# Kernel tuning notes

Measured on AMD Instinct MI355X. Metric: run time of the kernel, lower is better.

The kernel has to match this reference:

```python
import jax, jax.numpy as jnp
import numpy as np

H = 32  # rnn/encoder/residual hidden dim
NEG = -1e9


def gru(x, h0, Wih, Whh, bih, bhh):
    # x: (B,T,D), h0: (B,H); torch GRU gate order [r,z,n]
    xp = jnp.swapaxes(x @ Wih.T + bih, 0, 1)  # (T,B,3H)

    def step(h, xt):
        gh = h @ Whh.T + bhh
        xr, xz, xn = jnp.split(xt, 3, axis=-1)
        hr, hz, hn = jnp.split(gh, 3, axis=-1)
        r = jax.nn.sigmoid(xr + hr)
        z = jax.nn.sigmoid(xz + hz)
        n = jnp.tanh(xn + r * hn)
        h_new = (1.0 - z) * n + z * h
        return h_new, h_new

    hT, ys = jax.lax.scan(step, h0, xp)
    return jnp.swapaxes(ys, 0, 1), hT  # (B,T,H), (B,H)


def setup_inputs():
    key = jax.random.key(0)
    ks = jax.random.split(key, 30)
    B, T = 2048, 128
    def lin(k, o, i):
        return jax.random.normal(k, (o, i), jnp.float32) / np.sqrt(i)
    inp = {}
    inp['obs'] = jax.random.normal(ks[0], (B, T, 15), jnp.float32)
    inp['rnn_state'] = jax.random.normal(ks[1], (1, B, 3 * H), jnp.float32)
    inp['enc_air_W'] = lin(ks[2], H, 7); inp['enc_air_b'] = jnp.zeros((H,), jnp.float32)
    inp['enc_m_W'] = lin(ks[3], H, 4); inp['enc_m_b'] = jnp.zeros((H,), jnp.float32)
    inp['air_Wih'] = lin(ks[4], 3 * H, H); inp['air_Whh'] = lin(ks[5], 3 * H, H)
    inp['air_bih'] = jnp.zeros((3 * H,), jnp.float32); inp['air_bhh'] = jnp.zeros((3 * H,), jnp.float32)
    inp['m_Wih'] = lin(ks[6], 3 * H, H); inp['m_Whh'] = lin(ks[7], 3 * H, H)
    inp['m_bih'] = jnp.zeros((3 * H,), jnp.float32); inp['m_bhh'] = jnp.zeros((3 * H,), jnp.float32)
    inp['attn_in_w'] = lin(ks[8], 3 * H, H); inp['attn_in_b'] = jnp.zeros((3 * H,), jnp.float32)
    inp['attn_out_w'] = lin(ks[9], H, H); inp['attn_out_b'] = jnp.zeros((H,), jnp.float32)
    inp['mlp_W0'] = lin(ks[10], 256, 2 * H); inp['mlp_b0'] = jnp.zeros((256,), jnp.float32)
    inp['mlp_W1'] = lin(ks[11], 256, 256); inp['mlp_b1'] = jnp.zeros((256,), jnp.float32)
    inp['out_W'] = lin(ks[12], 1, 256); inp['out_b'] = jnp.zeros((1,), jnp.float32)
    return inp


def reference(obs, rnn_state, enc_air_W, enc_air_b, enc_m_W, enc_m_b,
              air_Wih, air_Whh, air_bih, air_bhh,
              m_Wih, m_Whh, m_bih, m_bhh,
              attn_in_w, attn_in_b, attn_out_w, attn_out_b,
              mlp_W0, mlp_b0, mlp_W1, mlp_b1, out_W, out_b):
    B, T, _ = obs.shape
    h_air0 = rnn_state[0, :, :H]                       # (B,H)
    h_m0 = rnn_state[0, :, H:].reshape(2 * B, H)       # faithful reshape (1,B,64)->(1,2B,32)

    # aircraft branch
    air_emb = obs[..., 8:] @ enc_air_W.T + enc_air_b   # (B,T,H)
    air_feat, next_h_air = gru(air_emb, h_air0, air_Wih, air_Whh, air_bih, air_bhh)

    # missile branch: concat missiles along batch dim
    m_raw = jnp.concatenate([obs[..., 0:4], obs[..., 4:8]], axis=0)  # (2B,T,4)
    m_emb = m_raw @ enc_m_W.T + enc_m_b
    m_feat, next_h_m = gru(m_emb, h_m0, m_Wih, m_Whh, m_bih, m_bhh)
    m1_feat, m2_feat = m_feat[:B], m_feat[B:]

    # inactive-missile mask from raw obs
    obs_flat = obs.reshape(-1, 15)
    inact = jnp.array([1.0, 0.0, 1.0, 0.0], jnp.float32)
    mask = jnp.stack([
        jnp.all(jnp.isclose(obs_flat[:, 0:4], inact), axis=-1),
        jnp.all(jnp.isclose(obs_flat[:, 4:8], inact), axis=-1),
    ], axis=1)                                          # (N,2) True = masked

    N = B * T
    air_flat = air_feat.reshape(N, H)
    m1_flat = m1_feat.reshape(N, H)
    m2_flat = m2_feat.reshape(N, H)

    # 2-head attention, q len 1, kv len 2
    Wq, Wk, Wv = jnp.split(attn_in_w, 3, axis=0)
    bq, bk, bv = jnp.split(attn_in_b, 3, axis=0)
    nh, hd = 2, H // 2
    qh = (air_flat @ Wq.T + bq).reshape(N, nh, hd)
    kv = jnp.stack([m1_flat, m2_flat], axis=1)          # (N,2,H)
    kh = (kv @ Wk.T + bk).reshape(N, 2, nh, hd)
    vh = (kv @ Wv.T + bv).reshape(N, 2, nh, hd)
    scores = jnp.einsum('nhd,nkhd->nhk', qh, kh) / np.sqrt(hd)
    scores = scores + jnp.where(mask[:, None, :], NEG, 0.0)
    w = jax.nn.softmax(scores, axis=-1)
    ctx = jnp.einsum('nhk,nkhd->nhd', w, vh).reshape(N, H)
    attn = ctx @ attn_out_w.T + attn_out_b
    attn = jnp.where(jnp.all(mask, axis=-1, keepdims=True), 0.0, attn)  # torch nan_to_num(all-masked)

    fusion = jnp.concatenate([air_flat, attn], axis=-1)  # (N,2H)
    h1 = jax.nn.leaky_relu(fusion @ mlp_W0.T + mlp_b0, 0.01)
    h2 = jax.nn.leaky_relu(h1 @ mlp_W1.T + mlp_b1, 0.01)
    val = h2 @ out_W.T + out_b                           # (N,1)

    next_h = jnp.concatenate([next_h_air, next_h_m.reshape(B, 2 * H)], axis=-1)[None]  # (1,B,96)
    return val, next_h
```

## Files before the change

kernel.cpp:

```cpp
#include <hip/hip_runtime.h>
#include <hip/hip_bf16.h>

#define BB 2048
#define TT 128
#define NN (BB*TT)
#define NVAL NN

#define OFF_W0P   2048u
#define OFF_W1P   10240u
#define OFF_WQKV  43008u
#define OFF_WO    44544u
#define OFF_PWHA  49792u
#define OFF_PWHM  51328u
#define OFF_PWCA  52864u
#define OFF_PWCM  54400u
#define OFF_BHNA  55936u
#define OFF_BHNM  55968u
#define OFF_AIRF  83968u
#define OFF_MF    4278272u
#define OFF_MASK  12666880u

#define L2E 1.44269504088896341f

typedef __attribute__((ext_vector_type(8))) short short8;
typedef __attribute__((ext_vector_type(4))) float f32x4;
typedef _Float16 f16x8 __attribute__((ext_vector_type(8)));
typedef unsigned u32x4 __attribute__((ext_vector_type(4)));

__device__ __forceinline__ unsigned short f2bf(float f) {
    unsigned u = __builtin_bit_cast(unsigned, f);
    u += 0x7FFFu + ((u >> 16) & 1u);
    return (unsigned short)(u >> 16);
}
__device__ __forceinline__ unsigned f2h(float f) {
    _Float16 h = (_Float16)f;
    return (unsigned)__builtin_bit_cast(unsigned short, h);
}
__device__ __forceinline__ unsigned pkh2(float a, float b) {
    return (f2h(b) << 16) | f2h(a);
}
__device__ __forceinline__ float fast_rcp(float x) {
    return __builtin_amdgcn_rcpf(x);
}
__device__ __forceinline__ float ex2(float x) {
    return __builtin_amdgcn_exp2f(x);
}
__device__ __forceinline__ unsigned cvt_pk_bf16(float a, float b) {
    unsigned r;
    asm("v_cvt_pk_bf16_f32 %0, %1, %2" : "=v"(r) : "v"(a), "v"(b));
    return r;
}
__device__ __forceinline__ f32x4 mfma16f(f16x8 a, f16x8 b, f32x4 c) {
    return __builtin_amdgcn_mfma_f32_16x16x32_f16(a, b, c, 0, 0, 0);
}
__device__ __forceinline__ f32x4 mfma16b(short8 a, short8 b, f32x4 c) {
    return __builtin_amdgcn_mfma_f32_16x16x32_bf16(a, b, c, 0, 0, 0);
}

__global__ __launch_bounds__(256) void prep_kernel(
    const float* __restrict__ enc_air_W, const float* __restrict__ enc_air_b,
    const float* __restrict__ enc_m_W,   const float* __restrict__ enc_m_b,
    const float* __restrict__ air_Wih,   const float* __restrict__ air_bih,
    const float* __restrict__ m_Wih,     const float* __restrict__ m_bih,
    const float* __restrict__ air_Whh,   const float* __restrict__ m_Whh,
    const float* __restrict__ air_bhh,   const float* __restrict__ m_bhh,
    const float* __restrict__ W0,        const float* __restrict__ W1,
    const float* __restrict__ attn_in_w, const float* __restrict__ attn_out_w,
    float* __restrict__ ws)
{
    int b = blockIdx.x, t = threadIdx.x;
    if (b == 0) {
    } else if (b <= 32) {
        unsigned short* w1p = (unsigned short*)(ws + OFF_W1P);
        int base = ((b-1)*256 + t);
        int lane = base & 63;
        int ctf  = base >> 6;
        int ct   = ctf & 15, s = ctf >> 4;
        int col = lane & 15, quad = lane >> 4;
        int k0 = s*32 + quad*8;
        int o  = ct*16 + col;
        #pragma unroll
        for (int j = 0; j < 8; j++)
            w1p[base*8 + j] = f2bf(W1[o*256 + k0 + j]);
    } else if (b <= 40) {
        unsigned short* w0p = (unsigned short*)(ws + OFF_W0P);
        int base = ((b-33)*256 + t);
        int lane = base & 63;
        int ctf  = base >> 6;
        int ct   = ctf & 15, s = ctf >> 4;
        int col = lane & 15, quad = lane >> 4;
        int k0 = s*32 + quad*8;
        int o  = ct*16 + col;
        #pragma unroll
        for (int j = 0; j < 8; j++)
            w0p[base*8 + j] = f2bf(W0[o*64 + k0 + j]);
    } else if (b == 41) {
        unsigned short* wqkv = (unsigned short*)(ws + OFF_WQKV);
        unsigned short* wop  = (unsigned short*)(ws + OFF_WO);
        for (int slot = t; slot < 512; slot += 256) {
            if (slot < 384) {
                int ct = slot >> 6, lane = slot & 63;
                int col = lane & 15, quad = lane >> 4;
                int o = ct*16 + col;
                #pragma unroll
                for (int j = 0; j < 8; j++)
                    wqkv[slot*8 + j] = f2bf(attn_in_w[o*32 + quad*8 + j]);
            } else {
                int s2 = slot - 384;
                int ct = s2 >> 6, lane = s2 & 63;
                int col = lane & 15, quad = lane >> 4;
                #pragma unroll
                for (int j = 0; j < 8; j++)
                    wop[s2*8 + j] = f2bf(attn_out_w[(ct*16+col)*32 + quad*8 + j]);
            }
        }
    } else if (b == 42) {
        unsigned* pa = (unsigned*)(ws + OFF_PWHA);
        unsigned* pm = (unsigned*)(ws + OFF_PWHM);
        for (int s = t; s < 3072; s += 256) {
            int s2 = (s < 1536) ? s : s - 1536;
            const float* W = (s < 1536) ? air_Whh : m_Whh;
            unsigned* dst = (s < 1536) ? pa : pm;
            int tile = s2 >> 8;
            int l    = (s2 >> 2) & 63;
            int d    = s2 & 3;
            int gate = tile >> 1, hfp = tile & 1;
            int rr = l & 15;
            int f  = (rr >> 2)*8 + hfp*4 + (rr & 3);
            int k  = (l >> 4)*8 + d*2;
            int row = gate*32 + f;
            float sc = (gate == 2) ? 2.f*L2E : L2E;
            dst[s2] = pkh2(W[row*32 + k]*sc, W[row*32 + k + 1]*sc);
        }
    } else {
        unsigned* pa = (unsigned*)(ws + OFF_PWCA);
        unsigned* pm = (unsigned*)(ws + OFF_PWCM);
        for (int s = t; s < 3072; s += 256) {
            bool isA = (s < 1536);
            int s2 = isA ? s : s - 1536;
            unsigned* dst = isA ? pa : pm;
            int tile = s2 >> 8, l = (s2 >> 2) & 63, d = s2 & 3;
            int gate = tile >> 1, hfp = tile & 1;
            int rr = l & 15;
            int f = (rr >> 2)*8 + hfp*4 + (rr & 3);
            int o = gate*32 + f;
            int kb = (l >> 4)*8 + d*2;
            int ni = isA ? 7 : 4;
            float sc = (gate == 2) ? 2.f*L2E : L2E;
            float v[2];
            #pragma unroll
            for (int e = 0; e < 2; e++) {
                int k = kb + e;
                float acc = 0.f;
                if (k < ni) {
                    for (int m = 0; m < 32; m++)
                        acc += isA ? air_Wih[o*32+m]*enc_air_W[m*7+k]
                                   : m_Wih[o*32+m]*enc_m_W[m*4+k];
                } else if (k == ni) {
                    acc = isA ? air_bih[o] : m_bih[o];
                    for (int m = 0; m < 32; m++)
                        acc += isA ? air_Wih[o*32+m]*enc_air_b[m]
                                   : m_Wih[o*32+m]*enc_m_b[m];
                    if (gate < 2) acc += isA ? air_bhh[o] : m_bhh[o];
                }
                v[e] = acc*sc;
            }
            dst[s2] = pkh2(v[0], v[1]);
        }
        if (t < 32) {
            ws[OFF_BHNA + t] = air_bhh[64 + t]*2.f*L2E;
            ws[OFF_BHNM + t] = m_bhh[64 + t]*2.f*L2E;
        }
    }
}

template<bool AIRT>
__device__ __forceinline__ void gru_tile(
    const float* __restrict__ obs, const float* __restrict__ rnn,
    const float* __restrict__ ws,
    unsigned short* __restrict__ feat, float* __restrict__ mask_f,
    float* __restrict__ nh_out, int tileIdx, unsigned* __restrict__ XH)
{
    const int lane = threadIdx.x & 63;
    const int col = lane & 15, quad = lane >> 4;

    const unsigned* pw = (const unsigned*)(ws + (AIRT ? OFF_PWHA : OFF_PWHM));
    const unsigned* pc = (const unsigned*)(ws + (AIRT ? OFF_PWCA : OFF_PWCM));
    f16x8 whf[6], wcf[6];
    #pragma unroll
    for (int i6 = 0; i6 < 6; i6++) {
        whf[i6] = __builtin_bit_cast(f16x8, *(const u32x4*)(pw + i6*256 + lane*4));
        wcf[i6] = __builtin_bit_cast(f16x8, *(const u32x4*)(pc + i6*256 + lane*4));
    }
    const float* bhnp = ws + (AIRT ? OFF_BHNA : OFF_BHNM) + quad*8;
    f32x4 bhn0 = *(const f32x4*)(bhnp);
    f32x4 bhn1 = *(const f32x4*)(bhnp + 4);

    int slot = 0, tb;
    if (AIRT) { tb = tileIdx*16; }
    else      { slot = tileIdx >> 7; tb = (tileIdx & 127)*16; }

    {
        const int coff = AIRT ? 8 : slot*4;
        #pragma unroll 4
        for (int it = 0; it < 32; it++) {
            int s = it*64 + lane;
            int r = s >> 7, t = s & 127;
            const float* p = obs + (size_t)(tb + r)*1920 + t*15 + coff;
            unsigned d0, d1, d2, d3;
            if (AIRT) {
                d0 = pkh2(p[0], p[1]); d1 = pkh2(p[2], p[3]);
                d2 = pkh2(p[4], p[5]); d3 = pkh2(p[6], 1.0f);
            } else {
                float x0 = p[0], x1 = p[1], x2 = p[2], x3 = p[3];
                d0 = pkh2(x0, x1); d1 = pkh2(x2, x3);
                d2 = 0x00003C00u; d3 = 0u;
                bool ok = (fabsf(x0 - 1.f) <= 1.00001e-5f) && (fabsf(x1) <= 1e-8f) &&
                          (fabsf(x2 - 1.f) <= 1.00001e-5f) && (fabsf(x3) <= 1e-8f);
                mask_f[((size_t)(tb + r)*TT + t)*2 + slot] = ok ? 1.f : 0.f;
            }
            unsigned off = (unsigned)(r*512 + 4*(t ^ (r & 7)));
            *(u32x4*)(XH + off) = (u32x4){d0, d1, d2, d3};
        }
    }
    __syncthreads();

    int rowi = tileIdx*16 + col;
    int hbase;
    if (AIRT) hbase = rowi*96;
    else      hbase = (rowi >> 1)*96 + 32 + (rowi & 1)*32;
    unsigned short* featp = feat + (size_t)rowi*(TT*32) + quad*8;

    f32x4 h0v = *(const f32x4*)(rnn + hbase + quad*8);
    f32x4 h1v = *(const f32x4*)(rnn + hbase + quad*8 + 4);

    const int xk = col & 7;
    const unsigned bidx = (unsigned)col*512;
    const f32x4 z4 = {0.f, 0.f, 0.f, 0.f};

    f32x4 gx0, gx1, gx2, gx3, gx4, gx5;
    {
        u32x4 xc = *(const u32x4*)(XH + bidx + 4u*(unsigned)(0 ^ xk));
        f16x8 xf = __builtin_bit_cast(f16x8, xc);
        gx0 = mfma16f(wcf[0], xf, z4); gx1 = mfma16f(wcf[1], xf, z4);
        gx2 = mfma16f(wcf[2], xf, z4); gx3 = mfma16f(wcf[3], xf, z4);
        gx4 = mfma16f(wcf[4], xf, z4); gx5 = mfma16f(wcf[5], xf, z4);
    }

    #pragma unroll 1
    for (int t = 0; t < TT; t++) {
        const int tn = (t < TT-1) ? t+1 : t;
        u32x4 xn = *(const u32x4*)(XH + bidx + 4u*(unsigned)(tn ^ xk));
        f16x8 xfn = __builtin_bit_cast(f16x8, xn);

        u32x4 hdv;
        hdv[0] = pkh2(h0v[0], h0v[1]); hdv[1] = pkh2(h0v[2], h0v[3]);
        hdv[2] = pkh2(h1v[0], h1v[1]); hdv[3] = pkh2(h1v[2], h1v[3]);
        f16x8 hff = __builtin_bit_cast(f16x8, hdv);

        f32x4 aR0 = mfma16f(whf[0], hff, gx0);
        f32x4 aR1 = mfma16f(whf[1], hff, gx1);
        f32x4 aZ0 = mfma16f(whf[2], hff, gx2);
        f32x4 aZ1 = mfma16f(whf[3], hff, gx3);
        f32x4 aHN0 = mfma16f(whf[4], hff, z4);
        f32x4 aHN1 = mfma16f(whf[5], hff, z4);
        f32x4 aXN0 = gx4, aXN1 = gx5;

        gx0 = mfma16f(wcf[0], xfn, z4); gx1 = mfma16f(wcf[1], xfn, z4);
        gx2 = mfma16f(wcf[2], xfn, z4); gx3 = mfma16f(wcf[3], xfn, z4);
        gx4 = mfma16f(wcf[4], xfn, z4); gx5 = mfma16f(wcf[5], xfn, z4);

        #pragma unroll
        for (int s = 0; s < 4; s++) {
            float er0 = ex2(-aR0[s]), ez0 = ex2(-aZ0[s]);
            float er1 = ex2(-aR1[s]), ez1 = ex2(-aZ1[s]);
            float pr0 = 1.f + er0, pz0 = 1.f + ez0;
            float pr1 = 1.f + er1, pz1 = 1.f + ez1;
            float d0 = pr0*pz0, d1 = pr1*pz1;
            float inv = fast_rcp(d0*d1);
            float t0 = d1*inv, t1 = d0*inv;
            float r0 = pz0*t0, zz0 = pr0*t0;
            float r1 = pz1*t1, zz1 = pr1*t1;
            float hn0 = aHN0[s] + bhn0[s];
            float hn1 = aHN1[s] + bhn1[s];
            float p0 = aXN0[s] + r0*hn0;
            float p1 = aXN1[s] + r1*hn1;
            float e20 = ex2(p0), e21 = ex2(p1);
            float q0 = e20 + 1.f, q1 = e21 + 1.f;
            float inv2 = fast_rcp(q0*q1);
            float n0 = 1.f - 2.f*(q1*inv2);
            float n1 = 1.f - 2.f*(q0*inv2);
            h0v[s] = n0 + zz0*(h0v[s] - n0);
            h1v[s] = n1 + zz1*(h1v[s] - n1);
        }

        u32x4 fw;
        fw[0] = cvt_pk_bf16(h0v[0], h0v[1]); fw[1] = cvt_pk_bf16(h0v[2], h0v[3]);
        fw[2] = cvt_pk_bf16(h1v[0], h1v[1]); fw[3] = cvt_pk_bf16(h1v[2], h1v[3]);
        *(u32x4*)(featp + (size_t)t*32) = fw;
    }
    *(f32x4*)(nh_out + hbase + quad*8)     = h0v;
    *(f32x4*)(nh_out + hbase + quad*8 + 4) = h1v;
}

__global__ __launch_bounds__(64, 1) void gru_kernel(
    const float* __restrict__ obs, const float* __restrict__ rnn,
    const float* __restrict__ ws,
    unsigned short* __restrict__ air_feat, unsigned short* __restrict__ m_feat,
    float* __restrict__ mask_f, float* __restrict__ nh_out)
{
    __shared__ unsigned XH[8192];
    int g = blockIdx.x;
    if (g < 128) gru_tile<true >(obs, rnn, ws, air_feat, mask_f, nh_out, g, XH);
    else         gru_tile<false>(obs, rnn, ws, m_feat,  mask_f, nh_out, g - 128, XH);
}

__global__ __launch_bounds__(512, 6) void fused_kernel(
    const unsigned short* __restrict__ air_feat, const unsigned short* __restrict__ m_feat,
    const float* __restrict__ mask_f,
    const unsigned short* __restrict__ wqkv, const float* __restrict__ attn_in_b,
    const unsigned short* __restrict__ wop,  const float* __restrict__ attn_out_b,
    const unsigned short* __restrict__ w0p, const float* __restrict__ b0,
    const unsigned short* __restrict__ w1p, const float* __restrict__ b1,
    const float* __restrict__ outW, const float* __restrict__ outb,
    float* __restrict__ val)
{
    __shared__ unsigned short A1[64*72];
    __shared__ unsigned short U[64*264];
    __shared__ float MS[128];
    __shared__ float PS[8][64];

    unsigned short* AM = U;
    unsigned short* CT = U + 64*72;
    unsigned short* A2 = U;

    const int tid  = threadIdx.x;
    const int lane = tid & 63;
    const int wid  = tid >> 6;
    const int col  = lane & 15;
    const int quad = lane >> 4;
    const size_t n0 = (size_t)blockIdx.x * 64;

    float b0r[2], b1r[2], owr[2];
    #pragma unroll
    for (int c = 0; c < 2; c++) {
        int ct = wid*2 + c;
        b0r[c] = b0[ct*16 + col];
        b1r[c] = b1[ct*16 + col];
        owr[c] = outW[ct*16 + col];
    }
    const float outb0 = outb[0];

    for (int s = tid; s < 768; s += 512) {
        int row = s & 63, part = (s >> 6) & 3, seg = s >> 8;
        int c0 = part*8;
        if (seg == 0) {
            short8 v = *(const short8*)(air_feat + (n0 + row)*32 + c0);
            *(short8*)&A1[row*72 + c0] = v;
        } else if (seg == 1) {
            short8 v = *(const short8*)(m_feat + (n0 + row)*32 + c0);
            *(short8*)&AM[row*72 + c0] = v;
        } else {
            short8 v = *(const short8*)(m_feat + ((size_t)NN + n0 + row)*32 + c0);
            *(short8*)&AM[row*72 + 32 + c0] = v;
        }
    }
    if (tid < 128) MS[tid] = mask_f[n0*2 + tid];
    __syncthreads();

    f32x4 acc1[4][2];
    #pragma unroll
    for (int s = 0; s < 4; s++)
        #pragma unroll
        for (int c = 0; c < 2; c++) acc1[s][c] = (f32x4){0.f,0.f,0.f,0.f};

    if (wid < 4) {
        const int strip = wid;
        short8 wqf[2], wkf[2], wvf[2], wof[2];
        #pragma unroll
        for (int ct = 0; ct < 2; ct++) {
            wqf[ct] = *(const short8*)(wqkv + ((0+ct)*64 + lane)*8);
            wkf[ct] = *(const short8*)(wqkv + ((2+ct)*64 + lane)*8);
            wvf[ct] = *(const short8*)(wqkv + ((4+ct)*64 + lane)*8);
            wof[ct] = *(const short8*)(wop + (ct*64 + lane)*8);
        }
        short8 a_air = *(const short8*)&A1[(strip*16 + col)*72 + quad*8];
        short8 a_m1  = *(const short8*)&AM[(strip*16 + col)*72 + quad*8];
        short8 a_m2  = *(const short8*)&AM[(strip*16 + col)*72 + 32 + quad*8];

        f32x4 q[2], k1[2], k2[2], v1[2], v2[2], ao[2];
        #pragma unroll
        for (int ct = 0; ct < 2; ct++) {
            f32x4 z = (f32x4){0.f,0.f,0.f,0.f};
            q[ct]  = mfma16b(a_air, wqf[ct], z);
            k1[ct] = mfma16b(a_m1,  wkf[ct], z);
            k2[ct] = mfma16b(a_m2,  wkf[ct], z);
            v1[ct] = mfma16b(a_m1,  wvf[ct], z);
            v2[ct] = mfma16b(a_m2,  wvf[ct], z);
        }
        float bqr[2], bkr[2], bvr[2];
        #pragma unroll
        for (int ct = 0; ct < 2; ct++) {
            bqr[ct] = attn_in_b[ct*16 + col];
            bkr[ct] = attn_in_b[32 + ct*16 + col];
            bvr[ct] = attn_in_b[64 + ct*16 + col];
        }
        float p1s[2][4], p2s[2][4];
        #pragma unroll
        for (int ct = 0; ct < 2; ct++) {
            #pragma unroll
            for (int reg = 0; reg < 4; reg++) {
                float qq = q[ct][reg] + bqr[ct];
                float p1 = qq * (k1[ct][reg] + bkr[ct]);
                float p2 = qq * (k2[ct][reg] + bkr[ct]);
                #pragma unroll
                for (int m = 1; m < 16; m <<= 1) {
                    p1 += __shfl_xor(p1, m, 64);
                    p2 += __shfl_xor(p2, m, 64);
                }
                p1s[ct][reg] = p1; p2s[ct][reg] = p2;
            }
        }
        float bothm[4];
        #pragma unroll
        for (int reg = 0; reg < 4; reg++) {
            int rloc = strip*16 + quad*4 + reg;
            float m0v = MS[rloc*2], m1v = MS[rloc*2 + 1];
            bothm[reg] = (m0v > 0.5f && m1v > 0.5f) ? 1.f : 0.f;
            #pragma unroll
            for (int ct = 0; ct < 2; ct++) {
                float s1 = p1s[ct][reg]*0.25f + (m0v > 0.5f ? -1e9f : 0.f);
                float s2 = p2s[ct][reg]*0.25f + (m1v > 0.5f ? -1e9f : 0.f);
                float mx = fmaxf(s1, s2);
                float e1 = __expf(s1 - mx), e2 = __expf(s2 - mx);
                float inv = fast_rcp(e1 + e2);
                float ctxv = ((v1[ct][reg] + bvr[ct])*e1 +
                              (v2[ct][reg] + bvr[ct])*e2) * inv;
                CT[rloc*40 + ct*16 + col] = f2bf(ctxv);
            }
        }
        short8 a_ctx = *(const short8*)&CT[(strip*16 + col)*40 + quad*8];
        #pragma unroll
        for (int ct = 0; ct < 2; ct++) {
            f32x4 z = (f32x4){0.f,0.f,0.f,0.f};
            ao[ct] = mfma16b(a_ctx, wof[ct], z);
        }
        float bor[2] = { attn_out_b[col], attn_out_b[16 + col] };
        #pragma unroll
        for (int reg = 0; reg < 4; reg++) {
            int rloc = strip*16 + quad*4 + reg;
            #pragma unroll
            for (int ct = 0; ct < 2; ct++) {
                float av = ao[ct][reg] + bor[ct];
                av = (bothm[reg] > 0.5f) ? 0.f : av;
                A1[rloc*72 + 32 + ct*16 + col] = f2bf(av);
            }
        }
    } else {
        short8 bfr[2], a0[4];
        #pragma unroll
        for (int c = 0; c < 2; c++)
            bfr[c] = *(const short8*)(w0p + ((wid*2 + c)*64 + lane)*8);
        #pragma unroll
        for (int s = 0; s < 4; s++)
            a0[s] = *(const short8*)&A1[(s*16 + col)*72 + quad*8];
        #pragma unroll
        for (int c = 0; c < 2; c++)
            #pragma unroll
            for (int s = 0; s < 4; s++)
                acc1[s][c] = mfma16b(a0[s], bfr[c], acc1[s][c]);
    }
    __syncthreads();

    if (wid < 4) {
        short8 bfr[2], a0[4];
        #pragma unroll
        for (int c = 0; c < 2; c++)
            bfr[c] = *(const short8*)(w0p + ((wid*2 + c)*64 + lane)*8);
        #pragma unroll
        for (int s = 0; s < 4; s++)
            a0[s] = *(const short8*)&A1[(s*16 + col)*72 + quad*8];
        #pragma unroll
        for (int c = 0; c < 2; c++)
            #pragma unroll
            for (int s = 0; s < 4; s++)
                acc1[s][c] = mfma16b(a0[s], bfr[c], acc1[s][c]);
    }
    {
        short8 bfr[2], a1f[4];
        #pragma unroll
        for (int c = 0; c < 2; c++)
            bfr[c] = *(const short8*)(w0p + ((16 + wid*2 + c)*64 + lane)*8);
        #pragma unroll
        for (int s = 0; s < 4; s++)
            a1f[s] = *(const short8*)&A1[(s*16 + col)*72 + 32 + quad*8];
        #pragma unroll
        for (int c = 0; c < 2; c++)
            #pragma unroll
            for (int s = 0; s < 4; s++)
                acc1[s][c] = mfma16b(a1f[s], bfr[c], acc1[s][c]);
    }
    __syncthreads();

    #pragma unroll
    for (int s = 0; s < 4; s++) {
        #pragma unroll
        for (int c = 0; c < 2; c++) {
            int ct = wid*2 + c;
            #pragma unroll
            for (int reg = 0; reg < 4; reg++) {
                float h = acc1[s][c][reg] + b0r[c];
                h = (h > 0.f) ? h : 0.01f*h;
                A2[(s*16 + quad*4 + reg)*264 + ct*16 + col] = f2bf(h);
            }
        }
    }
    __syncthreads();

    f32x4 acc2[4][2];
    #pragma unroll
    for (int s = 0; s < 4; s++)
        #pragma unroll
        for (int c = 0; c < 2; c++) acc2[s][c] = (f32x4){0.f,0.f,0.f,0.f};
    {
        short8 bfr[2], nbfr[2];
        #pragma unroll
        for (int c = 0; c < 2; c++)
            bfr[c] = *(const short8*)(w1p + ((0*16 + wid*2 + c)*64 + lane)*8);
        #pragma unroll
        for (int ks = 0; ks < 8; ks++) {
            if (ks < 7) {
                #pragma unroll
                for (int c = 0; c < 2; c++)
                    nbfr[c] = *(const short8*)(w1p + (((ks+1)*16 + wid*2 + c)*64 + lane)*8);
            }
            short8 a[4];
            #pragma unroll
            for (int s = 0; s < 4; s++)
                a[s] = *(const short8*)&A2[(s*16 + col)*264 + ks*32 + quad*8];
            #pragma unroll
            for (int c = 0; c < 2; c++)
                #pragma unroll
                for (int s = 0; s < 4; s++)
                    acc2[s][c] = mfma16b(a[s], bfr[c], acc2[s][c]);
            #pragma unroll
            for (int c = 0; c < 2; c++) bfr[c] = nbfr[c];
        }
    }

    #pragma unroll
    for (int s = 0; s < 4; s++) {
        float pv[4];
        #pragma unroll
        for (int reg = 0; reg < 4; reg++) pv[reg] = 0.f;
        #pragma unroll
        for (int c = 0; c < 2; c++) {
            #pragma unroll
            for (int reg = 0; reg < 4; reg++) {
                float h = acc2[s][c][reg] + b1r[c];
                h = (h > 0.f) ? h : 0.01f*h;
                pv[reg] += h*owr[c];
            }
        }
        #pragma unroll
        for (int reg = 0; reg < 4; reg++) {
            #pragma unroll
            for (int m = 1; m < 16; m <<= 1)
                pv[reg] += __shfl_xor(pv[reg], m, 64);
            if (col == 0) PS[wid][s*16 + quad*4 + reg] = pv[reg];
        }
    }
    __syncthreads();
    if (tid < 64)
        val[n0 + tid] = PS[0][tid] + PS[1][tid] + PS[2][tid] + PS[3][tid]
                      + PS[4][tid] + PS[5][tid] + PS[6][tid] + PS[7][tid] + outb0;
}

extern "C" void kernel_launch(void* const* d_in, const int* in_sizes, int n_in,
                              void* d_out, int out_size, void* d_ws, size_t ws_size,
                              hipStream_t stream) {
    const float* obs        = (const float*)d_in[0];
    const float* rnn        = (const float*)d_in[1];
    const float* enc_air_W  = (const float*)d_in[2];
    const float* enc_air_b  = (const float*)d_in[3];
    const float* enc_m_W    = (const float*)d_in[4];
    const float* enc_m_b    = (const float*)d_in[5];
    const float* air_Wih    = (const float*)d_in[6];
    const float* air_Whh    = (const float*)d_in[7];
    const float* air_bih    = (const float*)d_in[8];
    const float* air_bhh    = (const float*)d_in[9];
    const float* m_Wih      = (const float*)d_in[10];
    const float* m_Whh      = (const float*)d_in[11];
    const float* m_bih      = (const float*)d_in[12];
    const float* m_bhh      = (const float*)d_in[13];
    const float* attn_in_w  = (const float*)d_in[14];
    const float* attn_in_b  = (const float*)d_in[15];
    const float* attn_out_w = (const float*)d_in[16];
    const float* attn_out_b = (const float*)d_in[17];
    const float* mlp_W0     = (const float*)d_in[18];
    const float* mlp_b0     = (const float*)d_in[19];
    const float* mlp_W1     = (const float*)d_in[20];
    const float* mlp_b1     = (const float*)d_in[21];
    const float* out_W      = (const float*)d_in[22];
    const float* out_b      = (const float*)d_in[23];

    float* ws  = (float*)d_ws;
    float* out = (float*)d_out;

    prep_kernel<<<44, 256, 0, stream>>>(enc_air_W, enc_air_b, enc_m_W, enc_m_b,
                                        air_Wih, air_bih, m_Wih, m_bih,
                                        air_Whh, m_Whh, air_bhh, m_bhh,
                                        mlp_W0, mlp_W1, attn_in_w, attn_out_w, ws);

    gru_kernel<<<384, 64, 0, stream>>>(obs, rnn, ws,
                                       (unsigned short*)(ws + OFF_AIRF),
                                       (unsigned short*)(ws + OFF_MF),
                                       ws + OFF_MASK, out + NVAL);

    fused_kernel<<<NN/64, 512, 0, stream>>>((const unsigned short*)(ws + OFF_AIRF),
                                            (const unsigned short*)(ws + OFF_MF),
                                            ws + OFF_MASK,
                                            (const unsigned short*)(ws + OFF_WQKV), attn_in_b,
                                            (const unsigned short*)(ws + OFF_WO),   attn_out_b,
                                            (const unsigned short*)(ws + OFF_W0P), mlp_b0,
                                            (const unsigned short*)(ws + OFF_W1P), mlp_b1,
                                            out_W, out_b, out);
}
```

Before: 308.4 us.

## Transpose MLP GEMMs so layer-1 output feeds layer-2 directly as MFMA fragments

The fused MLP now computes the transposed products, with weights as the A operand and activations as the B operand. Layer-1 results are packed straight into the B-fragment layout of layer 2, and the W1 prep permutes its K ordering to match. Input features and mask are read from global memory directly into registers rather than staged in LDS. The layer-2 epilogue reduces with two cross-lane shuffles in place of four. Together these cut LDS staging, bank-conflicting scattered stores and shuffle work, but raise register use, and the occupancy hint drops from 6 to 4 blocks.

```diff
diff --git a/kernel.cpp b/kernel.cpp
--- a/kernel.cpp
+++ b/kernel.cpp
@@ -55,6 +55,9 @@
 }
 __device__ __forceinline__ f32x4 mfma16b(short8 a, short8 b, f32x4 c) {
     return __builtin_amdgcn_mfma_f32_16x16x32_bf16(a, b, c, 0, 0, 0);
+}
+__device__ __forceinline__ float lrelu(float h) {
+    return (h > 0.f) ? h : 0.01f*h;
 }
 
 __global__ __launch_bounds__(256) void prep_kernel(
@@ -75,13 +78,14 @@
         int base = ((b-1)*256 + t);
         int lane = base & 63;
         int ctf  = base >> 6;
-        int ct   = ctf & 15, s = ctf >> 4;
+        int ft2  = ctf & 15, kap = ctf >> 4;
         int col = lane & 15, quad = lane >> 4;
-        int k0 = s*32 + quad*8;
-        int o  = ct*16 + col;
-        #pragma unroll
-        for (int j = 0; j < 8; j++)
-            w1p[base*8 + j] = f2bf(W1[o*256 + k0 + j]);
+        int o  = ft2*16 + col;
+        #pragma unroll
+        for (int j = 0; j < 8; j++) {
+            int f = (2*kap + (j>>2))*16 + quad*4 + (j&3);
+            w1p[base*8 + j] = f2bf(W1[o*256 + f]);
+        }
     } else if (b <= 40) {
         unsigned short* w0p = (unsigned short*)(ws + OFF_W0P);
         int base = ((b-33)*256 + t);
@@ -315,7 +319,7 @@
     else         gru_tile<false>(obs, rnn, ws, m_feat,  mask_f, nh_out, g - 128, XH);
 }
 
-__global__ __launch_bounds__(512, 6) void fused_kernel(
+__global__ __launch_bounds__(512, 4) void fused_kernel(
     const unsigned short* __restrict__ air_feat, const unsigned short* __restrict__ m_feat,
     const float* __restrict__ mask_f,
     const unsigned short* __restrict__ wqkv, const float* __restrict__ attn_in_b,
@@ -325,14 +329,11 @@
     const float* __restrict__ outW, const float* __restrict__ outb,
     float* __restrict__ val)
 {
-    __shared__ unsigned short A1[64*72];
-    __shared__ unsigned short U[64*264];
-    __shared__ float MS[128];
+    __shared__ unsigned short XB[16384];
+    __shared__ unsigned short AT[4096];
     __shared__ float PS[8][64];
 
-    unsigned short* AM = U;
-    unsigned short* CT = U + 64*72;
-    unsigned short* A2 = U;
+    unsigned short* CT = XB;
 
     const int tid  = threadIdx.x;
     const int lane = tid & 63;
@@ -340,39 +341,18 @@
     const int col  = lane & 15;
     const int quad = lane >> 4;
     const size_t n0 = (size_t)blockIdx.x * 64;
-
-    float b0r[2], b1r[2], owr[2];
-    #pragma unroll
-    for (int c = 0; c < 2; c++) {
-        int ct = wid*2 + c;
-        b0r[c] = b0[ct*16 + col];
-        b1r[c] = b1[ct*16 + col];
-        owr[c] = outW[ct*16 + col];
-    }
-    const float outb0 = outb[0];
-
-    for (int s = tid; s < 768; s += 512) {
-        int row = s & 63, part = (s >> 6) & 3, seg = s >> 8;
-        int c0 = part*8;
-        if (seg == 0) {
-            short8 v = *(const short8*)(air_feat + (n0 + row)*32 + c0);
-            *(short8*)&A1[row*72 + c0] = v;
-        } else if (seg == 1) {
-            short8 v = *(const short8*)(m_feat + (n0 + row)*32 + c0);
-            *(short8*)&AM[row*72 + c0] = v;
-        } else {
-            short8 v = *(const short8*)(m_feat + ((size_t)NN + n0 + row)*32 + c0);
-            *(short8*)&AM[row*72 + 32 + c0] = v;
-        }
-    }
-    if (tid < 128) MS[tid] = mask_f[n0*2 + tid];
-    __syncthreads();
-
-    f32x4 acc1[4][2];
-    #pragma unroll
-    for (int s = 0; s < 4; s++)
-        #pragma unroll
-        for (int c = 0; c < 2; c++) acc1[s][c] = (f32x4){0.f,0.f,0.f,0.f};
+    const int rt    = wid & 3;
+    const int tbase = (wid >> 2) * 8;
+
+    short8 w0f0[8];
+    #pragma unroll
+    for (int i = 0; i < 8; i++)
+        w0f0[i] = *(const short8*)(w0p + ((tbase + i)*64 + lane)*8);
+    short8 bAir = *(const short8*)(air_feat + (n0 + rt*16 + col)*32 + quad*8);
+
+    f32x4 accL1[8];
+    #pragma unroll
+    for (int i = 0; i < 8; i++) accL1[i] = (f32x4){0.f,0.f,0.f,0.f};
 
     if (wid < 4) {
         const int strip = wid;
@@ -384,19 +364,25 @@
             wvf[ct] = *(const short8*)(wqkv + ((4+ct)*64 + lane)*8);
             wof[ct] = *(const short8*)(wop + (ct*64 + lane)*8);
         }
-        short8 a_air = *(const short8*)&A1[(strip*16 + col)*72 + quad*8];
-        short8 a_m1  = *(const short8*)&AM[(strip*16 + col)*72 + quad*8];
-        short8 a_m2  = *(const short8*)&AM[(strip*16 + col)*72 + 32 + quad*8];
+        short8 a_m1 = *(const short8*)(m_feat + (n0 + strip*16 + col)*32 + quad*8);
+        short8 a_m2 = *(const short8*)(m_feat + ((size_t)NN + n0 + strip*16 + col)*32 + quad*8);
+
+        float m0a[4], m1a[4];
+        #pragma unroll
+        for (int reg = 0; reg < 4; reg++) {
+            const float* mp = mask_f + (size_t)(n0 + strip*16 + quad*4 + reg)*2;
+            m0a[reg] = mp[0]; m1a[reg] = mp[1];
+        }
 
         f32x4 q[2], k1[2], k2[2], v1[2], v2[2], ao[2];
         #pragma unroll
         for (int ct = 0; ct < 2; ct++) {
             f32x4 z = (f32x4){0.f,0.f,0.f,0.f};
-            q[ct]  = mfma16b(a_air, wqf[ct], z);
-            k1[ct] = mfma16b(a_m1,  wkf[ct], z);
-            k2[ct] = mfma16b(a_m2,  wkf[ct], z);
-            v1[ct] = mfma16b(a_m1,  wvf[ct], z);
-            v2[ct] = mfma16b(a_m2,  wvf[ct], z);
+            q[ct]  = mfma16b(bAir, wqf[ct], z);
+            k1[ct] = mfma16b(a_m1, wkf[ct], z);
+            k2[ct] = mfma16b(a_m2, wkf[ct], z);
+            v1[ct] = mfma16b(a_m1, wvf[ct], z);
+            v2[ct] = mfma16b(a_m2, wvf[ct], z);
         }
         float bqr[2], bkr[2], bvr[2];
         #pragma unroll
@@ -425,7 +411,7 @@
         #pragma unroll
         for (int reg = 0; reg < 4; reg++) {
             int rloc = strip*16 + quad*4 + reg;
-            float m0v = MS[rloc*2], m1v = MS[rloc*2 + 1];
+            float m0v = m0a[reg], m1v = m1a[reg];
             bothm[reg] = (m0v > 0.5f && m1v > 0.5f) ? 1.f : 0.f;
             #pragma unroll
             for (int ct = 0; ct < 2; ct++) {
@@ -448,127 +434,102 @@
         float bor[2] = { attn_out_b[col], attn_out_b[16 + col] };
         #pragma unroll
         for (int reg = 0; reg < 4; reg++) {
-            int rloc = strip*16 + quad*4 + reg;
             #pragma unroll
             for (int ct = 0; ct < 2; ct++) {
                 float av = ao[ct][reg] + bor[ct];
                 av = (bothm[reg] > 0.5f) ? 0.f : av;
-                A1[rloc*72 + 32 + ct*16 + col] = f2bf(av);
+                AT[strip*1024 + (quad*4 + reg)*64 + ct*16 + col] = f2bf(av);
             }
         }
     } else {
-        short8 bfr[2], a0[4];
+        #pragma unroll
+        for (int i = 0; i < 8; i++)
+            accL1[i] = mfma16b(w0f0[i], bAir, accL1[i]);
+    }
+    __syncthreads();
+
+    if (wid < 4) {
+        #pragma unroll
+        for (int i = 0; i < 8; i++)
+            accL1[i] = mfma16b(w0f0[i], bAir, accL1[i]);
+    }
+    {
+        short8 bAttn = *(const short8*)&AT[rt*1024 + col*64 + quad*8];
+        #pragma unroll
+        for (int i = 0; i < 8; i++) {
+            short8 w0f1 = *(const short8*)(w0p + ((16 + tbase + i)*64 + lane)*8);
+            accL1[i] = mfma16b(w0f1, bAttn, accL1[i]);
+        }
+    }
+    #pragma unroll
+    for (int i = 0; i < 8; i += 2) {
+        int t0 = tbase + i;
+        f32x4 bA = *(const f32x4*)(b0 + t0*16 + quad*4);
+        f32x4 bB = *(const f32x4*)(b0 + (t0+1)*16 + quad*4);
+        float a0 = lrelu(accL1[i][0]   + bA[0]), a1 = lrelu(accL1[i][1]   + bA[1]);
+        float a2 = lrelu(accL1[i][2]   + bA[2]), a3 = lrelu(accL1[i][3]   + bA[3]);
+        float c0 = lrelu(accL1[i+1][0] + bB[0]), c1 = lrelu(accL1[i+1][1] + bB[1]);
+        float c2 = lrelu(accL1[i+1][2] + bB[2]), c3 = lrelu(accL1[i+1][3] + bB[3]);
+        u32x4 w;
+        w[0] = cvt_pk_bf16(a0, a1); w[1] = cvt_pk_bf16(a2, a3);
+        w[2] = cvt_pk_bf16(c0, c1); w[3] = cvt_pk_bf16(c2, c3);
+        int kap = t0 >> 1;
+        *(u32x4*)((unsigned*)XB + ((rt*8 + kap)*64 + lane)*4) = w;
+    }
+    __syncthreads();
+
+    f32x4 acc2[4][2];
+    #pragma unroll
+    for (int r = 0; r < 4; r++)
+        #pragma unroll
+        for (int c = 0; c < 2; c++) acc2[r][c] = (f32x4){0.f,0.f,0.f,0.f};
+    {
+        short8 w1f[2], w1n[2];
         #pragma unroll
         for (int c = 0; c < 2; c++)
-            bfr[c] = *(const short8*)(w0p + ((wid*2 + c)*64 + lane)*8);
-        #pragma unroll
-        for (int s = 0; s < 4; s++)
-            a0[s] = *(const short8*)&A1[(s*16 + col)*72 + quad*8];
-        #pragma unroll
-        for (int c = 0; c < 2; c++)
-            #pragma unroll
-            for (int s = 0; s < 4; s++)
-                acc1[s][c] = mfma16b(a0[s], bfr[c], acc1[s][c]);
-    }
-    __syncthreads();
-
-    if (wid < 4) {
-        short8 bfr[2], a0[4];
-        #pragma unroll
-        for (int c = 0; c < 2; c++)
-            bfr[c] = *(const short8*)(w0p + ((wid*2 + c)*64 + lane)*8);
-        #pragma unroll
-        for (int s = 0; s < 4; s++)
-            a0[s] = *(const short8*)&A1[(s*16 + col)*72 + quad*8];
-        #pragma unroll
-        for (int c = 0; c < 2; c++)
-            #pragma unroll
-            for (int s = 0; s < 4; s++)
-                acc1[s][c] = mfma16b(a0[s], bfr[c], acc1[s][c]);
-    }
-    {
-        short8 bfr[2], a1f[4];
-        #pragma unroll
-        for (int c = 0; c < 2; c++)
-            bfr[c] = *(const short8*)(w0p + ((16 + wid*2 + c)*64 + lane)*8);
-        #pragma unroll
-        for (int s = 0; s < 4; s++)
-            a1f[s] = *(const short8*)&A1[(s*16 + col)*72 + 32 + quad*8];
-        #pragma unroll
-        for (int c = 0; c < 2; c++)
-            #pragma unroll
-            for (int s = 0; s < 4; s++)
-                acc1[s][c] = mfma16b(a1f[s], bfr[c], acc1[s][c]);
-    }
-    __syncthreads();
-
-    #pragma unroll
-    for (int s = 0; s < 4; s++) {
-        #pragma unroll
-        for (int c = 0; c < 2; c++) {
-            int ct = wid*2 + c;
-            #pragma unroll
-            for (int reg = 0; reg < 4; reg++) {
-                float h = acc1[s][c][reg] + b0r[c];
-                h = (h > 0.f) ? h : 0.01f*h;
-                A2[(s*16 + quad*4 + reg)*264 + ct*16 + col] = f2bf(h);
-            }
-        }
-    }
-    __syncthreads();
-
-    f32x4 acc2[4][2];
-    #pragma unroll
-    for (int s = 0; s < 4; s++)
-        #pragma unroll
-        for (int c = 0; c < 2; c++) acc2[s][c] = (f32x4){0.f,0.f,0.f,0.f};
-    {
-        short8 bfr[2], nbfr[2];
-        #pragma unroll
-        for (int c = 0; c < 2; c++)
-            bfr[c] = *(const short8*)(w1p + ((0*16 + wid*2 + c)*64 + lane)*8);
-        #pragma unroll
-        for (int ks = 0; ks < 8; ks++) {
-            if (ks < 7) {
+            w1f[c] = *(const short8*)(w1p + ((0*16 + wid*2 + c)*64 + lane)*8);
+        #pragma unroll
+        for (int kap = 0; kap < 8; kap++) {
+            if (kap < 7) {
                 #pragma unroll
                 for (int c = 0; c < 2; c++)
-                    nbfr[c] = *(const short8*)(w1p + (((ks+1)*16 + wid*2 + c)*64 + lane)*8);
-            }
-            short8 a[4];
-            #pragma unroll
-            for (int s = 0; s < 4; s++)
-                a[s] = *(const short8*)&A2[(s*16 + col)*264 + ks*32 + quad*8];
+                    w1n[c] = *(const short8*)(w1p + (((kap+1)*16 + wid*2 + c)*64 + lane)*8);
+            }
+            short8 bx[4];
+            #pragma unroll
+            for (int r = 0; r < 4; r++)
+                bx[r] = *(const short8*)&XB[((r*8 + kap)*64 + lane)*8];
             #pragma unroll
             for (int c = 0; c < 2; c++)
                 #pragma unroll
-                for (int s = 0; s < 4; s++)
-                    acc2[s][c] = mfma16b(a[s], bfr[c], acc2[s][c]);
-            #pragma unroll
-            for (int c = 0; c < 2; c++) bfr[c] = nbfr[c];
-        }
-    }
-
-    #pragma unroll
-    for (int s = 0; s < 4; s++) {
-        float pv[4];
-        #pragma unroll
-        for (int reg = 0; reg < 4; reg++) pv[reg] = 0.f;
+                for (int r = 0; r < 4; r++)
+                    acc2[r][c] = mfma16b(w1f[c], bx[r], acc2[r][c]);
+            #pragma unroll
+            for (int c = 0; c < 2; c++) w1f[c] = w1n[c];
+        }
+    }
+
+    f32x4 b1v[2], owv[2];
+    #pragma unroll
+    for (int c = 0; c < 2; c++) {
+        b1v[c] = *(const f32x4*)(b1 + (wid*2 + c)*16 + quad*4);
+        owv[c] = *(const f32x4*)(outW + (wid*2 + c)*16 + quad*4);
+    }
+    const float outb0 = outb[0];
+    #pragma unroll
+    for (int r = 0; r < 4; r++) {
+        float pv = 0.f;
         #pragma unroll
         for (int c = 0; c < 2; c++) {
             #pragma unroll
             for (int reg = 0; reg < 4; reg++) {
-                float h = acc2[s][c][reg] + b1r[c];
-                h = (h > 0.f) ? h : 0.01f*h;
-                pv[reg] += h*owr[c];
-            }
-        }
-        #pragma unroll
-        for (int reg = 0; reg < 4; reg++) {
-            #pragma unroll
-            for (int m = 1; m < 16; m <<= 1)
-                pv[reg] += __shfl_xor(pv[reg], m, 64);
-            if (col == 0) PS[wid][s*16 + quad*4 + reg] = pv[reg];
-        }
+                float h = lrelu(acc2[r][c][reg] + b1v[c][reg]);
+                pv += h*owv[c][reg];
+            }
+        }
+        pv += __shfl_xor(pv, 16, 64);
+        pv += __shfl_xor(pv, 32, 64);
+        if (lane < 16) PS[wid][r*16 + lane] = pv;
     }
     __syncthreads();
     if (tid < 64)
```

Measured after the change: 304.7 us. About the same (-1.2%).
